# Kernel optimization log

Measured on AMD Instinct MI355X. Metric: run time of the kernel, lower is better.

## Reference

```python
import jax, jax.numpy as jnp
import numpy as np

N_NODES = 100000
N_EDGES = 600000
D_IN = 128
D_OUT = 96
N_REL = 4


def setup_inputs() -> dict:
    key = jax.random.key(0)
    ks = jax.random.split(key, 9)
    s = 1.0 / np.sqrt(D_IN)
    return {
        "classic_features": jax.random.normal(ks[0], (N_NODES, D_IN), jnp.float32),
        "edge_index": jax.random.randint(ks[1], (2, N_EDGES), 0, N_NODES),
        "edge_type": jax.random.randint(ks[2], (N_EDGES,), 0, N_REL),
        "W1": jax.random.uniform(ks[3], (N_REL, D_IN, D_IN), jnp.float32, -s, s),
        "root1": jax.random.uniform(ks[4], (D_IN, D_IN), jnp.float32, -s, s),
        "b1": jnp.zeros((D_IN,), jnp.float32),
        "W2": jax.random.uniform(ks[5], (N_REL, D_IN, D_OUT), jnp.float32, -s, s),
        "root2": jax.random.uniform(ks[6], (D_IN, D_OUT), jnp.float32, -s, s),
        "b2": jnp.zeros((D_OUT,), jnp.float32),
    }


def _rgcn_layer(x, src, dst, etype, W, root, b):
    # x: [N, d_in]; W: [R, d_in, d_out]
    n = x.shape[0]
    r = W.shape[0]
    # relation-specific transform of all nodes: [R, N, d_out]
    H = jnp.einsum('nd,rde->rne', x, W)
    msgs = H[etype, src]  # [E, d_out] gather per-edge transformed source feature
    # per-relation in-degree for mean aggregation (PyG RGCNConv mean norm)
    cnt = jnp.zeros((n, r), x.dtype).at[dst, etype].add(1.0)
    norm = 1.0 / jnp.maximum(cnt[dst, etype], 1.0)  # [E]
    agg = jnp.zeros((n, W.shape[-1]), x.dtype).at[dst].add(norm[:, None] * msgs)
    return agg + x @ root + b


def reference(classic_features, edge_index, edge_type, W1, root1, b1, W2, root2, b2):
    src, dst = edge_index[0], edge_index[1]
    h = _rgcn_layer(classic_features, src, dst, edge_type, W1, root1, b1)
    h = jax.nn.relu(h)  # dropout is identity in eval mode
    out = _rgcn_layer(h, src, dst, edge_type, W2, root2, b2)
    return out
```

## Files before the change

kernel.cpp:

```cpp
#include <hip/hip_runtime.h>

#define NN 100000
#define NE 600000
#define D  128
#define DOUT2 96
#define NREL 4
#define KREL 512
#define KCAT 640
#define SCAN_B 98

typedef short short8 __attribute__((ext_vector_type(8)));
typedef float f32x4  __attribute__((ext_vector_type(4)));

__device__ __forceinline__ ushort f2bf(float x) {
    unsigned u = __builtin_bit_cast(unsigned, x);
    u += 0x7fffu + ((u >> 16) & 1u);
    return (ushort)(u >> 16);
}
__device__ __forceinline__ float bfhi(unsigned u) {
    return __builtin_bit_cast(float, u & 0xffff0000u);
}
__device__ __forceinline__ float bflo(unsigned u) {
    return __builtin_bit_cast(float, u << 16);
}

__global__ void prep0(const float* __restrict__ x, ushort* __restrict__ Xb,
                      const float* __restrict__ W1, const float* __restrict__ root1,
                      short* __restrict__ Wp1,
                      const float* __restrict__ W2, const float* __restrict__ root2,
                      short* __restrict__ Wp2,
                      float* __restrict__ cnt, int* __restrict__ fill) {
    int i = blockIdx.x * 256 + threadIdx.x;
    const int S0 = (NN * NREL) / 4;
    const int S1 = NN / 4;
    const int S2 = (NN * D) / 4;
    const int S3 = KCAT * D;
    const int S4 = KCAT * DOUT2;
    if (i < S0) { ((float4*)cnt)[i] = make_float4(0.f, 0.f, 0.f, 0.f); return; }
    i -= S0;
    if (i < S1) { ((int4*)fill)[i] = make_int4(0, 0, 0, 0); return; }
    i -= S1;
    if (i < S2) {
        float4 v = ((const float4*)x)[i];
        ushort4 o;
        o.x = f2bf(v.x); o.y = f2bf(v.y); o.z = f2bf(v.z); o.w = f2bf(v.w);
        ((ushort4*)Xb)[i] = o;
        return;
    }
    i -= S2;
    if (i < S3) {
        int j = i & 7, rest = i >> 3;
        int n = rest % D, kq = rest / D;
        int k = kq * 8 + j;
        float v = (k < KREL) ? W1[(size_t)k * D + n] : root1[(size_t)(k - KREL) * D + n];
        Wp1[i] = (short)f2bf(v);
        return;
    }
    i -= S3;
    if (i < S4) {
        int j = i & 7, rest = i >> 3;
        int n = rest % DOUT2, kq = rest / DOUT2;
        int k = kq * 8 + j;
        float v = (k < KREL) ? W2[(size_t)k * DOUT2 + n] : root2[(size_t)(k - KREL) * DOUT2 + n];
        Wp2[i] = (short)f2bf(v);
        return;
    }
}

__global__ void count_deg(const int* __restrict__ dst,
                          const int* __restrict__ et,
                          float* __restrict__ cnt) {
    int e = blockIdx.x * blockDim.x + threadIdx.x;
    if (e < NE) unsafeAtomicAdd(&cnt[dst[e] * NREL + et[e]], 1.0f);
}

__global__ void scan1(const float* __restrict__ cnt, int* __restrict__ bsum) {
    __shared__ int s[256];
    int tid = threadIdx.x;
    int base = blockIdx.x * 1024 + tid * 4;
    int t = 0;
    for (int i = 0; i < 4; i++) {
        int v = base + i;
        if (v < NN) {
            float4 c = *(const float4*)&cnt[(size_t)v * 4];
            t += (int)(c.x + c.y + c.z + c.w);
        }
    }
    s[tid] = t; __syncthreads();
    for (int o = 128; o > 0; o >>= 1) {
        if (tid < o) s[tid] += s[tid + o];
        __syncthreads();
    }
    if (tid == 0) bsum[blockIdx.x] = s[0];
}

__global__ void scan2(int* __restrict__ bsum) {
    __shared__ int s[128];
    int tid = threadIdx.x;
    int mine = (tid < SCAN_B) ? bsum[tid] : 0;
    s[tid] = mine; __syncthreads();
    for (int o = 1; o < 128; o <<= 1) {
        int v = (tid >= o) ? s[tid - o] : 0;
        __syncthreads();
        s[tid] += v;
        __syncthreads();
    }
    if (tid < SCAN_B) bsum[tid] = s[tid] - mine;
}

__global__ void scan3(const float* __restrict__ cnt, const int* __restrict__ bsum,
                      int* __restrict__ off) {
    __shared__ int s[256];
    int tid = threadIdx.x;
    int base = blockIdx.x * 1024 + tid * 4;
    int d[4]; int t = 0;
    for (int i = 0; i < 4; i++) {
        int v = base + i; d[i] = 0;
        if (v < NN) {
            float4 c = *(const float4*)&cnt[(size_t)v * 4];
            d[i] = (int)(c.x + c.y + c.z + c.w);
        }
        t += d[i];
    }
    int mine = t;
    s[tid] = t; __syncthreads();
    for (int o = 1; o < 256; o <<= 1) {
        int v = (tid >= o) ? s[tid - o] : 0;
        __syncthreads();
        s[tid] += v;
        __syncthreads();
    }
    int ex = s[tid] - mine + bsum[blockIdx.x];
    for (int i = 0; i < 4; i++) {
        int v = base + i;
        if (v < NN) { off[v] = ex; ex += d[i]; }
    }
    if (blockIdx.x == 0 && tid == 0) off[NN] = NE;
}

__global__ void bucket_edges(const int* __restrict__ src, const int* __restrict__ dst,
                             const int* __restrict__ et, const int* __restrict__ off,
                             int* __restrict__ fill, int* __restrict__ srcpk) {
    int e = blockIdx.x * blockDim.x + threadIdx.x;
    if (e >= NE) return;
    int dn = dst[e];
    int pos = off[dn] + atomicAdd(&fill[dn], 1);
    srcpk[pos] = (src[e] << 2) | et[e];
}

template <int BN, bool RELU, bool OUT_BF16>
__global__ __launch_bounds__(256, 5) void rgcn_fused(
    const ushort* __restrict__ Xb,
    const int*   __restrict__ srcpk,
    const int*   __restrict__ off,
    const float* __restrict__ cnt,
    const short* __restrict__ Wcp,
    const float* __restrict__ bias,
    void*        __restrict__ Cout,
    int M) {
    constexpr int NFW = (BN / 16 + 1) / 2;
    __shared__ short At[64 * 32 * 8];

    const int tid  = threadIdx.x;
    const int wave = tid >> 6;
    const int lane = tid & 63;
    const int l    = lane & 15;
    const int qw   = lane >> 4;
    const int g    = wave * 4 + qw;
    const int v0   = blockIdx.x * 32;

#pragma unroll
    for (int half = 0; half < 2; half++) {
        int nv = g + half * 16;
        int v  = v0 + nv;
        float acc[4][8];
#pragma unroll
        for (int r = 0; r < 4; r++)
#pragma unroll
            for (int j = 0; j < 8; j++) acc[r][j] = 0.0f;

        float4 c4 = *(const float4*)&cnt[(size_t)v * 4];
        float nrm0 = 1.0f / fmaxf(c4.x, 1.0f);
        float nrm1 = 1.0f / fmaxf(c4.y, 1.0f);
        float nrm2 = 1.0f / fmaxf(c4.z, 1.0f);
        float nrm3 = 1.0f / fmaxf(c4.w, 1.0f);
        int e = off[v], end = off[v + 1];

#define EDGE_ACC(PK, XB) {                                                  \
        int t_ = (PK) & 3;                                                  \
        float s0 = (t_ == 0) ? nrm0 : 0.0f;                                 \
        float s1 = (t_ == 1) ? nrm1 : 0.0f;                                 \
        float s2 = (t_ == 2) ? nrm2 : 0.0f;                                 \
        float s3 = (t_ == 3) ? nrm3 : 0.0f;                                 \
        float xf[8];                                                        \
        xf[0] = bflo(XB.x); xf[1] = bfhi(XB.x);                             \
        xf[2] = bflo(XB.y); xf[3] = bfhi(XB.y);                             \
        xf[4] = bflo(XB.z); xf[5] = bfhi(XB.z);                             \
        xf[6] = bflo(XB.w); xf[7] = bfhi(XB.w);                             \
        _Pragma("unroll")                                                   \
        for (int j = 0; j < 8; j++) {                                       \
            acc[0][j] += s0 * xf[j];                                        \
            acc[1][j] += s1 * xf[j];                                        \
            acc[2][j] += s2 * xf[j];                                        \
            acc[3][j] += s3 * xf[j];                                        \
        } }

        for (; e + 3 < end; e += 4) {
            int p0 = srcpk[e],     p1 = srcpk[e + 1];
            int p2 = srcpk[e + 2], p3 = srcpk[e + 3];
            uint4 x0 = *(const uint4*)&Xb[(size_t)(p0 >> 2) * D + l * 8];
            uint4 x1 = *(const uint4*)&Xb[(size_t)(p1 >> 2) * D + l * 8];
            uint4 x2 = *(const uint4*)&Xb[(size_t)(p2 >> 2) * D + l * 8];
            uint4 x3 = *(const uint4*)&Xb[(size_t)(p3 >> 2) * D + l * 8];
            EDGE_ACC(p0, x0); EDGE_ACC(p1, x1);
            EDGE_ACC(p2, x2); EDGE_ACC(p3, x3);
        }
        for (; e < end; e++) {
            int p0 = srcpk[e];
            uint4 x0 = *(const uint4*)&Xb[(size_t)(p0 >> 2) * D + l * 8];
            EDGE_ACC(p0, x0);
        }
#undef EDGE_ACC

#pragma unroll
        for (int r = 0; r < 4; r++) {
            short8 w;
#pragma unroll
            for (int j = 0; j < 8; j++) w[j] = (short)f2bf(acc[r][j]);
            *(short8*)&At[((r * 16 + l) * 32 + nv) * 8] = w;
        }
    }

    __syncthreads();

    const int m16   = l;
    const int q     = qw;
    const int mt    = wave & 1;
    const int nbase = (wave >> 1) * NFW * 16;
    f32x4 acc2[NFW];
#pragma unroll
    for (int i = 0; i < NFW; i++) acc2[i] = (f32x4)0.0f;

#pragma unroll 4
    for (int ks = 0; ks < 16; ks++) {
        short8 af = *(const short8*)&At[((ks * 4 + q) * 32 + mt * 16 + m16) * 8];
        const short* bbase = Wcp + ((size_t)(ks * 4 + q) * BN + nbase + m16) * 8;
#pragma unroll
        for (int nf = 0; nf < NFW; nf++) {
            short8 bf = *(const short8*)(bbase + nf * 128);
            acc2[nf] = __builtin_amdgcn_mfma_f32_16x16x32_bf16(af, bf, acc2[nf], 0, 0, 0);
        }
    }
    {
        int rowc = v0 + mt * 16 + m16;
        const ushort* Xrow = Xb + (size_t)rowc * D;
#pragma unroll
        for (int s2 = 0; s2 < 4; s2++) {
            short8 af = *(const short8*)&Xrow[s2 * 32 + q * 8];
            const short* bbase = Wcp + ((size_t)((16 + s2) * 4 + q) * BN + nbase + m16) * 8;
#pragma unroll
            for (int nf = 0; nf < NFW; nf++) {
                short8 bf = *(const short8*)(bbase + nf * 128);
                acc2[nf] = __builtin_amdgcn_mfma_f32_16x16x32_bf16(af, bf, acc2[nf], 0, 0, 0);
            }
        }
    }

#pragma unroll
    for (int nf = 0; nf < NFW; nf++) {
        int n = nbase + nf * 16 + m16;
        float b = bias[n];
#pragma unroll
        for (int r = 0; r < 4; r++) {
            int m = v0 + mt * 16 + q * 4 + r;
            float vv = acc2[nf][r] + b;
            if (RELU) vv = fmaxf(vv, 0.0f);
            if (OUT_BF16) ((ushort*)Cout)[(size_t)m * BN + n] = f2bf(vv);
            else          ((float*)Cout)[(size_t)m * BN + n]  = vv;
        }
    }
}

extern "C" void kernel_launch(void* const* d_in, const int* in_sizes, int n_in,
                              void* d_out, int out_size, void* d_ws, size_t ws_size,
                              hipStream_t stream) {
    const float* x     = (const float*)d_in[0];
    const int*   ei    = (const int*)d_in[1];
    const int*   et    = (const int*)d_in[2];
    const float* W1    = (const float*)d_in[3];
    const float* root1 = (const float*)d_in[4];
    const float* b1    = (const float*)d_in[5];
    const float* W2    = (const float*)d_in[6];
    const float* root2 = (const float*)d_in[7];
    const float* b2    = (const float*)d_in[8];
    const int* srcp = ei;
    const int* dstp = ei + NE;
    float* out = (float*)d_out;

    short*  Wp1  = (short*)d_ws;
    short*  Wp2  = Wp1 + (size_t)KCAT * D;
    ushort* Xb   = (ushort*)(Wp2 + (size_t)KCAT * DOUT2);
    ushort* h    = Xb + (size_t)NN * D;
    float*  cnt  = (float*)(h + (size_t)NN * D);
    int*    off  = (int*)(cnt + (size_t)NN * NREL);
    int*    fill = off + (NN + 1);
    int*    bsum = fill + NN;
    int*    srcpk= bsum + 128;

    {
        const int S = (NN * NREL) / 4 + NN / 4 + (NN * D) / 4 + KCAT * D + KCAT * DOUT2;
        prep0<<<(S + 255) / 256, 256, 0, stream>>>(x, Xb, W1, root1, Wp1,
                                                   W2, root2, Wp2, cnt, fill);
    }
    count_deg<<<(NE + 255) / 256, 256, 0, stream>>>(dstp, et, cnt);
    scan1<<<SCAN_B, 256, 0, stream>>>(cnt, bsum);
    scan2<<<1, 128, 0, stream>>>(bsum);
    scan3<<<SCAN_B, 256, 0, stream>>>(cnt, bsum, off);
    bucket_edges<<<(NE + 255) / 256, 256, 0, stream>>>(srcp, dstp, et, off, fill, srcpk);

    const int fblocks = NN / 32;

    rgcn_fused<128, true, true><<<fblocks, 256, 0, stream>>>(
        Xb, srcpk, off, cnt, Wp1, b1, h, NN);
    rgcn_fused<96, false, false><<<fblocks, 256, 0, stream>>>(
        h, srcpk, off, cnt, Wp2, b2, out, NN);
}
```

Measured before the change: 327.0 us.

## Precompute per-edge norms, unroll gather by 8, swizzle LDS, overlap root MFMA

Bucketing now stores each edge's mean-normalisation factor next to its packed source and type, so the fused layer no longer loads cnt or computes reciprocals per node. The gather loop is unrolled to 8 edges with a branch-reduced tail of up to 3 edges, and accumulation uses packed float2 math. LDS writes and reads of the aggregated tile use an XOR swizzle to reduce bank conflicts. The root-weight MFMA is moved ahead of the barrier so it overlaps with waves still aggregating. The cost is a doubled edge array size and more registers, which may reduce occupancy.

```diff
diff --git a/kernel.cpp b/kernel.cpp
--- a/kernel.cpp
+++ b/kernel.cpp
@@ -11,17 +11,18 @@
 
 typedef short short8 __attribute__((ext_vector_type(8)));
 typedef float f32x4  __attribute__((ext_vector_type(4)));
+typedef float f32x2  __attribute__((ext_vector_type(2)));
 
 __device__ __forceinline__ ushort f2bf(float x) {
     unsigned u = __builtin_bit_cast(unsigned, x);
     u += 0x7fffu + ((u >> 16) & 1u);
     return (ushort)(u >> 16);
 }
-__device__ __forceinline__ float bfhi(unsigned u) {
-    return __builtin_bit_cast(float, u & 0xffff0000u);
-}
-__device__ __forceinline__ float bflo(unsigned u) {
-    return __builtin_bit_cast(float, u << 16);
+__device__ __forceinline__ f32x2 bfpair(unsigned u) {
+    f32x2 r;
+    r.x = __builtin_bit_cast(float, u << 16);
+    r.y = __builtin_bit_cast(float, u & 0xffff0000u);
+    return r;
 }
 
 __global__ void prep0(const float* __restrict__ x, ushort* __restrict__ Xb,
@@ -140,20 +141,22 @@
 
 __global__ void bucket_edges(const int* __restrict__ src, const int* __restrict__ dst,
                              const int* __restrict__ et, const int* __restrict__ off,
-                             int* __restrict__ fill, int* __restrict__ srcpk) {
+                             int* __restrict__ fill, int2* __restrict__ epk,
+                             const float* __restrict__ cnt) {
     int e = blockIdx.x * blockDim.x + threadIdx.x;
     if (e >= NE) return;
     int dn = dst[e];
+    int t  = et[e];
     int pos = off[dn] + atomicAdd(&fill[dn], 1);
-    srcpk[pos] = (src[e] << 2) | et[e];
+    float nrm = 1.0f / fmaxf(cnt[dn * NREL + t], 1.0f);
+    epk[pos] = make_int2((src[e] << 2) | t, __builtin_bit_cast(int, nrm));
 }
 
 template <int BN, bool RELU, bool OUT_BF16>
 __global__ __launch_bounds__(256, 5) void rgcn_fused(
     const ushort* __restrict__ Xb,
-    const int*   __restrict__ srcpk,
+    const int2*  __restrict__ epk,
     const int*   __restrict__ off,
-    const float* __restrict__ cnt,
     const short* __restrict__ Wcp,
     const float* __restrict__ bias,
     void*        __restrict__ Cout,
@@ -170,55 +173,73 @@
     const int v0   = blockIdx.x * 32;
 
 #pragma unroll
-    for (int half = 0; half < 2; half++) {
-        int nv = g + half * 16;
+    for (int hf = 0; hf < 2; hf++) {
+        int nv = g + hf * 16;
         int v  = v0 + nv;
-        float acc[4][8];
+        f32x2 acc[4][4];
 #pragma unroll
         for (int r = 0; r < 4; r++)
 #pragma unroll
-            for (int j = 0; j < 8; j++) acc[r][j] = 0.0f;
-
-        float4 c4 = *(const float4*)&cnt[(size_t)v * 4];
-        float nrm0 = 1.0f / fmaxf(c4.x, 1.0f);
-        float nrm1 = 1.0f / fmaxf(c4.y, 1.0f);
-        float nrm2 = 1.0f / fmaxf(c4.z, 1.0f);
-        float nrm3 = 1.0f / fmaxf(c4.w, 1.0f);
+            for (int k = 0; k < 4; k++) acc[r][k] = (f32x2)0.0f;
+
         int e = off[v], end = off[v + 1];
 
-#define EDGE_ACC(PK, XB) {                                                  \
+#define EDGE_ACC(PK, SF, XB) {                                              \
         int t_ = (PK) & 3;                                                  \
-        float s0 = (t_ == 0) ? nrm0 : 0.0f;                                 \
-        float s1 = (t_ == 1) ? nrm1 : 0.0f;                                 \
-        float s2 = (t_ == 2) ? nrm2 : 0.0f;                                 \
-        float s3 = (t_ == 3) ? nrm3 : 0.0f;                                 \
-        float xf[8];                                                        \
-        xf[0] = bflo(XB.x); xf[1] = bfhi(XB.x);                             \
-        xf[2] = bflo(XB.y); xf[3] = bfhi(XB.y);                             \
-        xf[4] = bflo(XB.z); xf[5] = bfhi(XB.z);                             \
-        xf[6] = bflo(XB.w); xf[7] = bfhi(XB.w);                             \
-        _Pragma("unroll")                                                   \
-        for (int j = 0; j < 8; j++) {                                       \
-            acc[0][j] += s0 * xf[j];                                        \
-            acc[1][j] += s1 * xf[j];                                        \
-            acc[2][j] += s2 * xf[j];                                        \
-            acc[3][j] += s3 * xf[j];                                        \
-        } }
-
+        float s0_ = (t_ == 0) ? (SF) : 0.0f;                                \
+        float s1_ = (t_ == 1) ? (SF) : 0.0f;                                \
+        float s2_ = (t_ == 2) ? (SF) : 0.0f;                                \
+        float s3_ = (t_ == 3) ? (SF) : 0.0f;                                \
+        f32x2 xp_;                                                          \
+        xp_ = bfpair((XB).x);                                               \
+        acc[0][0] += s0_ * xp_; acc[1][0] += s1_ * xp_;                     \
+        acc[2][0] += s2_ * xp_; acc[3][0] += s3_ * xp_;                     \
+        xp_ = bfpair((XB).y);                                               \
+        acc[0][1] += s0_ * xp_; acc[1][1] += s1_ * xp_;                     \
+        acc[2][1] += s2_ * xp_; acc[3][1] += s3_ * xp_;                     \
+        xp_ = bfpair((XB).z);                                               \
+        acc[0][2] += s0_ * xp_; acc[1][2] += s1_ * xp_;                     \
+        acc[2][2] += s2_ * xp_; acc[3][2] += s3_ * xp_;                     \
+        xp_ = bfpair((XB).w);                                               \
+        acc[0][3] += s0_ * xp_; acc[1][3] += s1_ * xp_;                     \
+        acc[2][3] += s2_ * xp_; acc[3][3] += s3_ * xp_; }
+
+        for (; e + 7 < end; e += 8) {
+            int2 ep[8];
+#pragma unroll
+            for (int k = 0; k < 8; k++) ep[k] = epk[e + k];
+            uint4 xv[8];
+#pragma unroll
+            for (int k = 0; k < 8; k++)
+                xv[k] = *(const uint4*)&Xb[(size_t)(ep[k].x >> 2) * D + l * 8];
+#pragma unroll
+            for (int k = 0; k < 8; k++)
+                EDGE_ACC(ep[k].x, __builtin_bit_cast(float, ep[k].y), xv[k]);
+        }
         for (; e + 3 < end; e += 4) {
-            int p0 = srcpk[e],     p1 = srcpk[e + 1];
-            int p2 = srcpk[e + 2], p3 = srcpk[e + 3];
-            uint4 x0 = *(const uint4*)&Xb[(size_t)(p0 >> 2) * D + l * 8];
-            uint4 x1 = *(const uint4*)&Xb[(size_t)(p1 >> 2) * D + l * 8];
-            uint4 x2 = *(const uint4*)&Xb[(size_t)(p2 >> 2) * D + l * 8];
-            uint4 x3 = *(const uint4*)&Xb[(size_t)(p3 >> 2) * D + l * 8];
-            EDGE_ACC(p0, x0); EDGE_ACC(p1, x1);
-            EDGE_ACC(p2, x2); EDGE_ACC(p3, x3);
-        }
-        for (; e < end; e++) {
-            int p0 = srcpk[e];
-            uint4 x0 = *(const uint4*)&Xb[(size_t)(p0 >> 2) * D + l * 8];
-            EDGE_ACC(p0, x0);
+            int2 ep[4];
+#pragma unroll
+            for (int k = 0; k < 4; k++) ep[k] = epk[e + k];
+            uint4 xv[4];
+#pragma unroll
+            for (int k = 0; k < 4; k++)
+                xv[k] = *(const uint4*)&Xb[(size_t)(ep[k].x >> 2) * D + l * 8];
+#pragma unroll
+            for (int k = 0; k < 4; k++)
+                EDGE_ACC(ep[k].x, __builtin_bit_cast(float, ep[k].y), xv[k]);
+        }
+        if (e < end) {
+            int rem = end - e;
+            int ea = e + (rem > 1);
+            int eb = e + ((rem > 2) ? 2 : 0);
+            int2 e0 = epk[e], e1 = epk[ea], e2 = epk[eb];
+            float f0 = __builtin_bit_cast(float, e0.y);
+            float f1 = (rem > 1) ? __builtin_bit_cast(float, e1.y) : 0.0f;
+            float f2 = (rem > 2) ? __builtin_bit_cast(float, e2.y) : 0.0f;
+            uint4 x0 = *(const uint4*)&Xb[(size_t)(e0.x >> 2) * D + l * 8];
+            uint4 x1 = *(const uint4*)&Xb[(size_t)(e1.x >> 2) * D + l * 8];
+            uint4 x2 = *(const uint4*)&Xb[(size_t)(e2.x >> 2) * D + l * 8];
+            EDGE_ACC(e0.x, f0, x0); EDGE_ACC(e1.x, f1, x1); EDGE_ACC(e2.x, f2, x2);
         }
 #undef EDGE_ACC
 
@@ -226,12 +247,14 @@
         for (int r = 0; r < 4; r++) {
             short8 w;
 #pragma unroll
-            for (int j = 0; j < 8; j++) w[j] = (short)f2bf(acc[r][j]);
-            *(short8*)&At[((r * 16 + l) * 32 + nv) * 8] = w;
-        }
-    }
-
-    __syncthreads();
+            for (int k = 0; k < 4; k++) {
+                w[2 * k]     = (short)f2bf(acc[r][k].x);
+                w[2 * k + 1] = (short)f2bf(acc[r][k].y);
+            }
+            int kq = r * 16 + l;
+            *(short8*)&At[(kq * 32 + (nv ^ (kq & 7))) * 8] = w;
+        }
+    }
 
     const int m16   = l;
     const int q     = qw;
@@ -241,16 +264,6 @@
 #pragma unroll
     for (int i = 0; i < NFW; i++) acc2[i] = (f32x4)0.0f;
 
-#pragma unroll 4
-    for (int ks = 0; ks < 16; ks++) {
-        short8 af = *(const short8*)&At[((ks * 4 + q) * 32 + mt * 16 + m16) * 8];
-        const short* bbase = Wcp + ((size_t)(ks * 4 + q) * BN + nbase + m16) * 8;
-#pragma unroll
-        for (int nf = 0; nf < NFW; nf++) {
-            short8 bf = *(const short8*)(bbase + nf * 128);
-            acc2[nf] = __builtin_amdgcn_mfma_f32_16x16x32_bf16(af, bf, acc2[nf], 0, 0, 0);
-        }
-    }
     {
         int rowc = v0 + mt * 16 + m16;
         const ushort* Xrow = Xb + (size_t)rowc * D;
@@ -263,6 +276,20 @@
                 short8 bf = *(const short8*)(bbase + nf * 128);
                 acc2[nf] = __builtin_amdgcn_mfma_f32_16x16x32_bf16(af, bf, acc2[nf], 0, 0, 0);
             }
+        }
+    }
+
+    __syncthreads();
+
+#pragma unroll 4
+    for (int ks = 0; ks < 16; ks++) {
+        int kq = ks * 4 + q;
+        short8 af = *(const short8*)&At[(kq * 32 + ((mt * 16 + m16) ^ (kq & 7))) * 8];
+        const short* bbase = Wcp + ((size_t)kq * BN + nbase + m16) * 8;
+#pragma unroll
+        for (int nf = 0; nf < NFW; nf++) {
+            short8 bf = *(const short8*)(bbase + nf * 128);
+            acc2[nf] = __builtin_amdgcn_mfma_f32_16x16x32_bf16(af, bf, acc2[nf], 0, 0, 0);
         }
     }
 
@@ -305,7 +332,7 @@
     int*    off  = (int*)(cnt + (size_t)NN * NREL);
     int*    fill = off + (NN + 1);
     int*    bsum = fill + NN;
-    int*    srcpk= bsum + 128;
+    int2*   epk  = (int2*)(bsum + 136);
 
     {
         const int S = (NN * NREL) / 4 + NN / 4 + (NN * D) / 4 + KCAT * D + KCAT * DOUT2;
@@ -316,12 +343,13 @@
     scan1<<<SCAN_B, 256, 0, stream>>>(cnt, bsum);
     scan2<<<1, 128, 0, stream>>>(bsum);
     scan3<<<SCAN_B, 256, 0, stream>>>(cnt, bsum, off);
-    bucket_edges<<<(NE + 255) / 256, 256, 0, stream>>>(srcp, dstp, et, off, fill, srcpk);
+    bucket_edges<<<(NE + 255) / 256, 256, 0, stream>>>(srcp, dstp, et, off, fill,
+                                                       epk, cnt);
 
     const int fblocks = NN / 32;
 
     rgcn_fused<128, true, true><<<fblocks, 256, 0, stream>>>(
-        Xb, srcpk, off, cnt, Wp1, b1, h, NN);
+        Xb, epk, off, Wp1, b1, h, NN);
     rgcn_fused<96, false, false><<<fblocks, 256, 0, stream>>>(
-        h, srcpk, off, cnt, Wp2, b2, out, NN);
-}
+        h, epk, off, Wp2, b2, out, NN);
+}
```

New measurement: 365.7 us. +11.8%, slower.
